# Performance work log

Measured on AMD Instinct MI355X. Metric: run time of the kernel, lower is better.

Reference implementation:

```python
import jax, jax.numpy as jnp
import numpy as np

L, B, D, H = 256, 128, 2048, 2048


def setup_inputs() -> dict:
    key = jax.random.key(0)
    k_x, k_ih, k_hh, k_b = jax.random.split(key, 4)
    scale_ih = 1.0 / np.sqrt(D)
    scale_hh = 1.0 / np.sqrt(H)
    return {
        "inputs": jax.random.normal(k_x, (L, B, D), dtype=jnp.float32),
        "W_ih": jax.random.normal(k_ih, (D, H), dtype=jnp.float32) * scale_ih,
        "W_hh": jax.random.normal(k_hh, (H, H), dtype=jnp.float32) * scale_hh,
        "b": jax.random.normal(k_b, (H,), dtype=jnp.float32) * scale_hh,
    }


def reference(inputs, W_ih, W_hh, b):
    """RNN.forward with a vanilla tanh cell, non-packed path, return_output=True.

    cell.forward(x, h) -> (h', h') with h' = tanh(x @ W_ih + h @ W_hh + b).
    default_state = zeros. Returns (stacked outputs [L,B,H], final state [B,H]).
    """
    # Hoist the input projection out of the scan (x @ W_ih is time-parallel).
    xp = jnp.einsum("lbd,dh->lbh", inputs, W_ih) + b  # [L, B, H]

    def step(h, x_t):
        h_new = jnp.tanh(x_t + h @ W_hh)  # [B, H]
        return h_new, h_new

    h0 = jnp.zeros((inputs.shape[1], W_hh.shape[0]), dtype=inputs.dtype)
    final_state, outputs = jax.lax.scan(step, h0, xp)
    return outputs, final_state
```

## Files before the change

### kernel.cpp

```cpp
#include <hip/hip_runtime.h>
#include <hip/hip_bf16.h>
#include <cmath>

#define LSEQ 256
#define BB   128
#define DD   2048
#define HH   2048
#define BH   (BB*HH)

typedef __attribute__((ext_vector_type(8))) short short8;
typedef __attribute__((ext_vector_type(4))) short short4v;
typedef __attribute__((ext_vector_type(4))) float f32x4;

__device__ __forceinline__ void split2(float x, short& hi, short& lo) {
    unsigned u = __float_as_uint(x);
    hi = (short)(u >> 16);
    float r = x - __uint_as_float(u & 0xffff0000u);
    lo = (short)(__float_as_uint(r) >> 16);
}

#define MFMA(a, b, c) __builtin_amdgcn_mfma_f32_16x16x32_bf16((a), (b), (c), 0, 0, 0)

__global__ __launch_bounds__(256) void transpose_split(const float* __restrict__ W,
                                                       short* __restrict__ outH,
                                                       short* __restrict__ outL) {
    __shared__ float S[64][65];
    const int tid = threadIdx.x;
    const int r0 = blockIdx.x * 64;
    const int c0 = blockIdx.y * 64;
    const int lr = tid >> 2;
    const int lc = (tid & 3) * 16;
#pragma unroll
    for (int j = 0; j < 4; ++j) {
        f32x4 v = *(const f32x4*)&W[(size_t)(r0 + lr) * DD + c0 + lc + 4*j];
#pragma unroll
        for (int q = 0; q < 4; ++q) S[lr][lc + 4*j + q] = v[q];
    }
    __syncthreads();
    short8 h8[2], l8[2];
#pragma unroll
    for (int j = 0; j < 16; ++j) {
        short h, l;
        split2(S[lc + j][lr], h, l);
        h8[j >> 3][j & 7] = h; l8[j >> 3][j & 7] = l;
    }
    const size_t o = (size_t)(c0 + lr) * DD + r0 + lc;
    *(short8*)&outH[o]     = h8[0];
    *(short8*)&outH[o + 8] = h8[1];
    *(short8*)&outL[o]     = l8[0];
    *(short8*)&outL[o + 8] = l8[1];
}

__global__ __launch_bounds__(256) void xp_gemm(const float* __restrict__ X,
                                               const short* __restrict__ WTh,
                                               const short* __restrict__ WTl,
                                               const float* __restrict__ bias,
                                               float* __restrict__ C,
                                               short* __restrict__ h0H,
                                               short* __restrict__ h0L) {
    __shared__ short Ah_s[128 * 40];
    __shared__ short Al_s[128 * 40];

    const int tid = threadIdx.x, lane = tid & 63, wave = tid >> 6;
    const int l15 = lane & 15, lg = lane >> 4;

    const int gid = blockIdx.x;
    const int rt = ((gid >> 8) << 4) | (gid & 15);
    const int ct = (gid >> 4) & 15;
    const int row0 = rt * 128, col0 = ct * 128;
    const int wm = (wave >> 1) * 64, wn = (wave & 1) * 64;

    const int sr = tid >> 3, sc = (tid & 7) * 4;
    const float* gA = X + (size_t)(row0 + sr) * DD + sc;

    size_t brow[4];
#pragma unroll
    for (int n = 0; n < 4; ++n)
        brow[n] = (size_t)(col0 + wn + n * 16 + l15) * DD + lg * 8;

    f32x4 acc[4][4] = {};

    for (int k0 = 0; k0 < DD; k0 += 32) {
        f32x4 av[4];
        short4v h4[4], l4[4];
#pragma unroll
        for (int i = 0; i < 4; ++i)
            av[i] = *(const f32x4*)(gA + (size_t)(32 * i) * DD + k0);
#pragma unroll
        for (int i = 0; i < 4; ++i)
#pragma unroll
            for (int q = 0; q < 4; ++q) {
                short h, l; split2(av[i][q], h, l);
                h4[i][q] = h; l4[i][q] = l;
            }
        short8 bh[4], bl[4];
#pragma unroll
        for (int n = 0; n < 4; ++n) {
            bh[n] = *(const short8*)&WTh[brow[n] + k0];
            bl[n] = *(const short8*)&WTl[brow[n] + k0];
        }
        __syncthreads();
#pragma unroll
        for (int i = 0; i < 4; ++i) {
            *(short4v*)&Ah_s[(sr + 32 * i) * 40 + sc] = h4[i];
            *(short4v*)&Al_s[(sr + 32 * i) * 40 + sc] = l4[i];
        }
        __syncthreads();
        short8 ah[4], al[4];
#pragma unroll
        for (int m = 0; m < 4; ++m) {
            const int ro = (wm + m * 16 + l15) * 40 + lg * 8;
            ah[m] = *(const short8*)&Ah_s[ro];
            al[m] = *(const short8*)&Al_s[ro];
        }
#pragma unroll
        for (int m = 0; m < 4; ++m)
#pragma unroll
            for (int n = 0; n < 4; ++n) {
                acc[m][n] = MFMA(ah[m], bh[n], acc[m][n]);
                acc[m][n] = MFMA(ah[m], bl[n], acc[m][n]);
                acc[m][n] = MFMA(al[m], bh[n], acc[m][n]);
            }
    }

    float bv[4];
#pragma unroll
    for (int n = 0; n < 4; ++n) bv[n] = bias[col0 + wn + n * 16 + l15];

    if (rt == 0) {
#pragma unroll
        for (int m = 0; m < 4; ++m)
#pragma unroll
            for (int n = 0; n < 4; ++n)
#pragma unroll
                for (int i = 0; i < 4; ++i) {
                    const int row = wm + m * 16 + lg * 4 + i;
                    const int col = col0 + wn + n * 16 + l15;
                    const float t = tanhf(acc[m][n][i] + bv[n]);
                    const size_t o = (size_t)row * HH + col;
                    C[o] = t;
                    short h, l; split2(t, h, l);
                    h0H[o] = h; h0L[o] = l;
                }
    } else {
#pragma unroll
        for (int m = 0; m < 4; ++m)
#pragma unroll
            for (int n = 0; n < 4; ++n)
#pragma unroll
                for (int i = 0; i < 4; ++i) {
                    const int row = row0 + wm + m * 16 + lg * 4 + i;
                    const int col = col0 + wn + n * 16 + l15;
                    C[(size_t)row * HH + col] = acc[m][n][i] + bv[n];
                }
    }
}

__global__ __launch_bounds__(256) void rnn_step(const short* __restrict__ hH,
                                                const short* __restrict__ hL,
                                                const short* __restrict__ WTh,
                                                const short* __restrict__ WTl,
                                                float* __restrict__ io,
                                                short* __restrict__ oH,
                                                short* __restrict__ oL) {
    __shared__ float red[4][32 * 32];

    const int tid = threadIdx.x, lane = tid & 63, wave = tid >> 6;
    const int l15 = lane & 15, lg = lane >> 4;
    const int mr = blockIdx.x >> 6, nc = blockIdx.x & 63;
    const int m0 = mr * 32, n0 = nc * 32;

    const size_t a0 = (size_t)(m0 + l15) * HH;
    const size_t a1 = a0 + (size_t)16 * HH;
    const size_t b0 = (size_t)(n0 + l15) * HH;
    const size_t b1 = b0 + (size_t)16 * HH;
    const int kb = wave * 512 + lg * 8;

    f32x4 acc[2][2] = {};
#pragma unroll
    for (int kt = 0; kt < 16; ++kt) {
        const int k = kb + kt * 32;
        const short8 ah0 = *(const short8*)&hH[a0 + k];
        const short8 ah1 = *(const short8*)&hH[a1 + k];
        const short8 al0 = *(const short8*)&hL[a0 + k];
        const short8 al1 = *(const short8*)&hL[a1 + k];
        const short8 bh0 = *(const short8*)&WTh[b0 + k];
        const short8 bh1 = *(const short8*)&WTh[b1 + k];
        const short8 bl0 = *(const short8*)&WTl[b0 + k];
        const short8 bl1 = *(const short8*)&WTl[b1 + k];

        acc[0][0] = MFMA(ah0, bh0, acc[0][0]);
        acc[0][0] = MFMA(ah0, bl0, acc[0][0]);
        acc[0][0] = MFMA(al0, bh0, acc[0][0]);

        acc[0][1] = MFMA(ah0, bh1, acc[0][1]);
        acc[0][1] = MFMA(ah0, bl1, acc[0][1]);
        acc[0][1] = MFMA(al0, bh1, acc[0][1]);

        acc[1][0] = MFMA(ah1, bh0, acc[1][0]);
        acc[1][0] = MFMA(ah1, bl0, acc[1][0]);
        acc[1][0] = MFMA(al1, bh0, acc[1][0]);

        acc[1][1] = MFMA(ah1, bh1, acc[1][1]);
        acc[1][1] = MFMA(ah1, bl1, acc[1][1]);
        acc[1][1] = MFMA(al1, bh1, acc[1][1]);
    }

#pragma unroll
    for (int m = 0; m < 2; ++m)
#pragma unroll
        for (int n = 0; n < 2; ++n)
#pragma unroll
            for (int i = 0; i < 4; ++i)
                red[wave][(m * 16 + lg * 4 + i) * 32 + n * 16 + l15] = acc[m][n][i];
    __syncthreads();

    const int r = tid >> 3, cb = (tid & 7) * 4;
    float* dst = io + (size_t)(m0 + r) * HH + n0 + cb;
    f32x4 xv = *(const f32x4*)dst;
    f32x4 ov;
    short4v h4, l4;
#pragma unroll
    for (int q = 0; q < 4; ++q) {
        const int c = r * 32 + cb + q;
        const float s = xv[q] + red[0][c] + red[1][c] + red[2][c] + red[3][c];
        const float t = tanhf(s);
        ov[q] = t;
        short h, l; split2(t, h, l);
        h4[q] = h; l4[q] = l;
    }
    *(f32x4*)dst = ov;
    const size_t po = (size_t)(m0 + r) * HH + n0 + cb;
    *(short4v*)&oH[po] = h4;
    *(short4v*)&oL[po] = l4;
}

extern "C" void kernel_launch(void* const* d_in, const int* in_sizes, int n_in,
                              void* d_out, int out_size, void* d_ws, size_t ws_size,
                              hipStream_t stream) {
    (void)in_sizes; (void)n_in; (void)out_size; (void)ws_size;

    const float* X   = (const float*)d_in[0];
    const float* Wih = (const float*)d_in[1];
    const float* Whh = (const float*)d_in[2];
    const float* b   = (const float*)d_in[3];
    float* out = (float*)d_out;

    char* ws = (char*)d_ws;
    short* WihTh = (short*)(ws);
    short* WihTl = (short*)(ws + (size_t) 8*1024*1024);
    short* WhhTh = (short*)(ws + (size_t)16*1024*1024);
    short* WhhTl = (short*)(ws + (size_t)24*1024*1024);
    short* hb[2][2];
    hb[0][0] = (short*)(ws + (size_t)32*1024*1024);
    hb[0][1] = (short*)(ws + (size_t)32*1024*1024 + 512*1024);
    hb[1][0] = (short*)(ws + (size_t)33*1024*1024);
    hb[1][1] = (short*)(ws + (size_t)33*1024*1024 + 512*1024);

    dim3 tg(32, 32);
    transpose_split<<<tg, 256, 0, stream>>>(Wih, WihTh, WihTl);
    transpose_split<<<tg, 256, 0, stream>>>(Whh, WhhTh, WhhTl);

    xp_gemm<<<4096, 256, 0, stream>>>(X, WihTh, WihTl, b, out, hb[0][0], hb[0][1]);

    for (int t = 1; t < LSEQ; ++t) {
        const int pi = (t - 1) & 1, po = t & 1;
        rnn_step<<<256, 256, 0, stream>>>(hb[pi][0], hb[pi][1], WhhTh, WhhTl,
                                          out + (size_t)t * BH, hb[po][0], hb[po][1]);
    }

    hipMemcpyAsync(out + (size_t)LSEQ * BH, out + (size_t)(LSEQ - 1) * BH,
                   (size_t)BH * sizeof(float), hipMemcpyDeviceToDevice, stream);
}
```

Measured before the change: 6.378 ms.

## Fuse recurrent steps into one persistent kernel with grid barrier and LDS-resident weights

Replaces the 255 per-timestep kernel launches with a single persistent kernel of 256 blocks that loops over time and synchronizes through a global atomic generation barrier. Each block keeps its 32-column slice of the high bf16 half of W_hh in swizzled shared memory (128KB), so only the low half is re-read from global memory each step. Blocks grow to 512 threads with a two-phase shared-memory reduction, and the final-state copy is folded into the last step. The approach relies on all 256 blocks being co-resident (one per CU) for the spin barrier to avoid deadlock, and uses a large LDS allocation per block.

```diff
diff --git a/kernel.cpp b/kernel.cpp
--- a/kernel.cpp
+++ b/kernel.cpp
@@ -7,6 +7,7 @@
 #define DD   2048
 #define HH   2048
 #define BH   (BB*HH)
+#define NBLK 256
 
 typedef __attribute__((ext_vector_type(8))) short short8;
 typedef __attribute__((ext_vector_type(4))) short short4v;
@@ -156,83 +157,128 @@
     }
 }
 
-__global__ __launch_bounds__(256) void rnn_step(const short* __restrict__ hH,
-                                                const short* __restrict__ hL,
-                                                const short* __restrict__ WTh,
+__global__ __launch_bounds__(512) void rnn_scan(const short* __restrict__ WTh,
                                                 const short* __restrict__ WTl,
-                                                float* __restrict__ io,
-                                                short* __restrict__ oH,
-                                                short* __restrict__ oL) {
-    __shared__ float red[4][32 * 32];
+                                                short* __restrict__ hA_hi, short* __restrict__ hA_lo,
+                                                short* __restrict__ hB_hi, short* __restrict__ hB_lo,
+                                                float* __restrict__ out,
+                                                float* __restrict__ final_state,
+                                                unsigned* barrier_cnt, unsigned* barrier_gen) {
+    __shared__ short Whi[32 * 2048];
+    __shared__ float red[4][1024];
 
     const int tid = threadIdx.x, lane = tid & 63, wave = tid >> 6;
     const int l15 = lane & 15, lg = lane >> 4;
     const int mr = blockIdx.x >> 6, nc = blockIdx.x & 63;
     const int m0 = mr * 32, n0 = nc * 32;
 
+    for (int it = 0; it < 16; ++it) {
+        const int ci  = it * 512 + tid;
+        const int col = ci >> 8;
+        const int kc  = ci & 255;
+        const short8 v = *(const short8*)&WTh[(size_t)(n0 + col) * HH + kc * 8];
+        const int byte = ((col << 12) + (kc << 4)) ^ ((col & 7) << 4);
+        *(short8*)((char*)Whi + byte) = v;
+    }
+    __syncthreads();
+
     const size_t a0 = (size_t)(m0 + l15) * HH;
     const size_t a1 = a0 + (size_t)16 * HH;
     const size_t b0 = (size_t)(n0 + l15) * HH;
     const size_t b1 = b0 + (size_t)16 * HH;
-    const int kb = wave * 512 + lg * 8;
-
-    f32x4 acc[2][2] = {};
-#pragma unroll
-    for (int kt = 0; kt < 16; ++kt) {
-        const int k = kb + kt * 32;
-        const short8 ah0 = *(const short8*)&hH[a0 + k];
-        const short8 ah1 = *(const short8*)&hH[a1 + k];
-        const short8 al0 = *(const short8*)&hL[a0 + k];
-        const short8 al1 = *(const short8*)&hL[a1 + k];
-        const short8 bh0 = *(const short8*)&WTh[b0 + k];
-        const short8 bh1 = *(const short8*)&WTh[b1 + k];
-        const short8 bl0 = *(const short8*)&WTl[b0 + k];
-        const short8 bl1 = *(const short8*)&WTl[b1 + k];
-
-        acc[0][0] = MFMA(ah0, bh0, acc[0][0]);
-        acc[0][0] = MFMA(ah0, bl0, acc[0][0]);
-        acc[0][0] = MFMA(al0, bh0, acc[0][0]);
-
-        acc[0][1] = MFMA(ah0, bh1, acc[0][1]);
-        acc[0][1] = MFMA(ah0, bl1, acc[0][1]);
-        acc[0][1] = MFMA(al0, bh1, acc[0][1]);
-
-        acc[1][0] = MFMA(ah1, bh0, acc[1][0]);
-        acc[1][0] = MFMA(ah1, bl0, acc[1][0]);
-        acc[1][0] = MFMA(al1, bh0, acc[1][0]);
-
-        acc[1][1] = MFMA(ah1, bh1, acc[1][1]);
-        acc[1][1] = MFMA(ah1, bl1, acc[1][1]);
-        acc[1][1] = MFMA(al1, bh1, acc[1][1]);
-    }
-
-#pragma unroll
-    for (int m = 0; m < 2; ++m)
-#pragma unroll
-        for (int n = 0; n < 2; ++n)
-#pragma unroll
-            for (int i = 0; i < 4; ++i)
-                red[wave][(m * 16 + lg * 4 + i) * 32 + n * 16 + l15] = acc[m][n][i];
-    __syncthreads();
-
-    const int r = tid >> 3, cb = (tid & 7) * 4;
-    float* dst = io + (size_t)(m0 + r) * HH + n0 + cb;
-    f32x4 xv = *(const f32x4*)dst;
-    f32x4 ov;
-    short4v h4, l4;
-#pragma unroll
-    for (int q = 0; q < 4; ++q) {
-        const int c = r * 32 + cb + q;
-        const float s = xv[q] + red[0][c] + red[1][c] + red[2][c] + red[3][c];
-        const float t = tanhf(s);
-        ov[q] = t;
-        short h, l; split2(t, h, l);
-        h4[q] = h; l4[q] = l;
-    }
-    *(f32x4*)dst = ov;
-    const size_t po = (size_t)(m0 + r) * HH + n0 + cb;
-    *(short4v*)&oH[po] = h4;
-    *(short4v*)&oL[po] = l4;
+    const int kbase = wave * 256 + lg * 8;
+    const int c0b = l15, c1b = 16 + l15;
+    const int colbase0 = c0b << 12, swz0 = (c0b & 7) << 4;
+    const int colbase1 = c1b << 12, swz1 = (c1b & 7) << 4;
+
+    const int e = tid * 2, er = e >> 5, ec = e & 31;
+    const size_t po = (size_t)(m0 + er) * HH + n0 + ec;
+
+    for (int t = 1; t < LSEQ; ++t) {
+        const short* hHp = (t & 1) ? hA_hi : hB_hi;
+        const short* hLp = (t & 1) ? hA_lo : hB_lo;
+        short* oH = (t & 1) ? hB_hi : hA_hi;
+        short* oL = (t & 1) ? hB_lo : hA_lo;
+        float* io = out + (size_t)t * BH;
+
+        f32x4 acc00 = {}, acc01 = {}, acc10 = {}, acc11 = {};
+#pragma unroll
+        for (int kt = 0; kt < 8; ++kt) {
+            const int k = kbase + kt * 32;
+            const short8 ah0 = *(const short8*)&hHp[a0 + k];
+            const short8 ah1 = *(const short8*)&hHp[a1 + k];
+            const short8 al0 = *(const short8*)&hLp[a0 + k];
+            const short8 al1 = *(const short8*)&hLp[a1 + k];
+            const short8 bl0 = *(const short8*)&WTl[b0 + k];
+            const short8 bl1 = *(const short8*)&WTl[b1 + k];
+            const short8 bh0 = *(const short8*)((const char*)Whi + (colbase0 | ((2 * k) ^ swz0)));
+            const short8 bh1 = *(const short8*)((const char*)Whi + (colbase1 | ((2 * k) ^ swz1)));
+
+            acc00 = MFMA(ah0, bh0, acc00); acc00 = MFMA(ah0, bl0, acc00); acc00 = MFMA(al0, bh0, acc00);
+            acc01 = MFMA(ah0, bh1, acc01); acc01 = MFMA(ah0, bl1, acc01); acc01 = MFMA(al0, bh1, acc01);
+            acc10 = MFMA(ah1, bh0, acc10); acc10 = MFMA(ah1, bl0, acc10); acc10 = MFMA(al1, bh0, acc10);
+            acc11 = MFMA(ah1, bh1, acc11); acc11 = MFMA(ah1, bl1, acc11); acc11 = MFMA(al1, bh1, acc11);
+        }
+
+        f32x4 am[2][2] = {{acc00, acc01}, {acc10, acc11}};
+        if (wave < 4) {
+#pragma unroll
+            for (int m = 0; m < 2; ++m)
+#pragma unroll
+                for (int n = 0; n < 2; ++n)
+#pragma unroll
+                    for (int i = 0; i < 4; ++i)
+                        red[wave][(m * 16 + lg * 4 + i) * 32 + n * 16 + l15] = am[m][n][i];
+        }
+        __syncthreads();
+        if (wave >= 4) {
+#pragma unroll
+            for (int m = 0; m < 2; ++m)
+#pragma unroll
+                for (int n = 0; n < 2; ++n)
+#pragma unroll
+                    for (int i = 0; i < 4; ++i)
+                        red[wave - 4][(m * 16 + lg * 4 + i) * 32 + n * 16 + l15] += am[m][n][i];
+        }
+        __syncthreads();
+
+        {
+            float* iop = io + po;
+            const float2 xv = *(const float2*)iop;
+            const int base = er * 32 + ec;
+            const float2 r0 = *(const float2*)&red[0][base];
+            const float2 r1 = *(const float2*)&red[1][base];
+            const float2 r2 = *(const float2*)&red[2][base];
+            const float2 r3 = *(const float2*)&red[3][base];
+            const float t0 = tanhf(xv.x + r0.x + r1.x + r2.x + r3.x);
+            const float t1 = tanhf(xv.y + r0.y + r1.y + r2.y + r3.y);
+            *(float2*)iop = make_float2(t0, t1);
+            short h0s, l0s, h1s, l1s;
+            split2(t0, h0s, l0s); split2(t1, h1s, l1s);
+            *(unsigned*)&oH[po] = (unsigned)(unsigned short)h0s | ((unsigned)(unsigned short)h1s << 16);
+            *(unsigned*)&oL[po] = (unsigned)(unsigned short)l0s | ((unsigned)(unsigned short)l1s << 16);
+            if (t == LSEQ - 1)
+                *(float2*)(final_state + po) = make_float2(t0, t1);
+        }
+
+        if (t != LSEQ - 1) {
+            __syncthreads();
+            if (tid == 0) {
+                __threadfence();
+                unsigned g = __hip_atomic_load(barrier_gen, __ATOMIC_ACQUIRE, __HIP_MEMORY_SCOPE_AGENT);
+                unsigned a = __hip_atomic_fetch_add(barrier_cnt, 1u, __ATOMIC_ACQ_REL, __HIP_MEMORY_SCOPE_AGENT);
+                if (a == NBLK - 1) {
+                    __hip_atomic_store(barrier_cnt, 0u, __ATOMIC_RELAXED, __HIP_MEMORY_SCOPE_AGENT);
+                    __hip_atomic_fetch_add(barrier_gen, 1u, __ATOMIC_RELEASE, __HIP_MEMORY_SCOPE_AGENT);
+                } else {
+                    while (__hip_atomic_load(barrier_gen, __ATOMIC_ACQUIRE, __HIP_MEMORY_SCOPE_AGENT) == g)
+                        __builtin_amdgcn_s_sleep(2);
+                }
+                __threadfence();
+            }
+            __syncthreads();
+        }
+    }
 }
 
 extern "C" void kernel_launch(void* const* d_in, const int* in_sizes, int n_in,
@@ -251,24 +297,20 @@
     short* WihTl = (short*)(ws + (size_t) 8*1024*1024);
     short* WhhTh = (short*)(ws + (size_t)16*1024*1024);
     short* WhhTl = (short*)(ws + (size_t)24*1024*1024);
-    short* hb[2][2];
-    hb[0][0] = (short*)(ws + (size_t)32*1024*1024);
-    hb[0][1] = (short*)(ws + (size_t)32*1024*1024 + 512*1024);
-    hb[1][0] = (short*)(ws + (size_t)33*1024*1024);
-    hb[1][1] = (short*)(ws + (size_t)33*1024*1024 + 512*1024);
+    short* hA_hi = (short*)(ws + (size_t)32*1024*1024);
+    short* hA_lo = (short*)(ws + (size_t)32*1024*1024 + 512*1024);
+    short* hB_hi = (short*)(ws + (size_t)33*1024*1024);
+    short* hB_lo = (short*)(ws + (size_t)33*1024*1024 + 512*1024);
+    unsigned* bar = (unsigned*)(ws + (size_t)34*1024*1024);
+
+    hipMemsetAsync(bar, 0, 2 * sizeof(unsigned), stream);
 
     dim3 tg(32, 32);
     transpose_split<<<tg, 256, 0, stream>>>(Wih, WihTh, WihTl);
     transpose_split<<<tg, 256, 0, stream>>>(Whh, WhhTh, WhhTl);
 
-    xp_gemm<<<4096, 256, 0, stream>>>(X, WihTh, WihTl, b, out, hb[0][0], hb[0][1]);
-
-    for (int t = 1; t < LSEQ; ++t) {
-        const int pi = (t - 1) & 1, po = t & 1;
-        rnn_step<<<256, 256, 0, stream>>>(hb[pi][0], hb[pi][1], WhhTh, WhhTl,
-                                          out + (size_t)t * BH, hb[po][0], hb[po][1]);
-    }
-
-    hipMemcpyAsync(out + (size_t)LSEQ * BH, out + (size_t)(LSEQ - 1) * BH,
-                   (size_t)BH * sizeof(float), hipMemcpyDeviceToDevice, stream);
-}
+    xp_gemm<<<4096, 256, 0, stream>>>(X, WihTh, WihTl, b, out, hA_hi, hA_lo);
+
+    rnn_scan<<<NBLK, 512, 0, stream>>>(WhhTh, WhhTl, hA_hi, hA_lo, hB_hi, hB_lo,
+                                       out, out + (size_t)LSEQ * BH, bar, bar + 1);
+}
```

Result: slower. 13.73 ms (+115.3%).
